# Optimization experiments

Measured on AMD Instinct MI355X. Metric: run time of the kernel, lower is better.

The kernel has to match this reference:

```python
import jax, jax.numpy as jnp
import numpy as np

STRIDE = 4
IMG_H, IMG_W = 800, 1216
NMS_THRESH = 0.7
PRE_NMS = 1000
POST_NMS = 1000
MIN_SIZE = 0.0
SCALE_CLAMP = float(np.log(1000.0 / 16.0))  # detectron2 Box2BoxTransform clamp
A = 3  # anchors per location


def _cell_anchors():
    size = 32.0
    ars = jnp.array([0.5, 1.0, 2.0], jnp.float32)
    area = size * size
    w = jnp.sqrt(area / ars)
    h = ars * w
    return jnp.stack([-w / 2, -h / 2, w / 2, h / 2], axis=1)  # [A,4]


def _anchors(H, W):
    sx = jnp.arange(W, dtype=jnp.float32) * STRIDE
    sy = jnp.arange(H, dtype=jnp.float32) * STRIDE
    gy, gx = jnp.meshgrid(sy, sx, indexing='ij')
    shifts = jnp.stack([gx, gy, gx, gy], axis=-1).reshape(-1, 1, 4)  # [H*W,1,4]
    return (shifts + _cell_anchors()[None]).reshape(-1, 4)  # [H*W*A,4]


def _conv(x, w, b, pad):
    y = jax.lax.conv_general_dilated(x, w, (1, 1), pad,
                                     dimension_numbers=('NCHW', 'OIHW', 'NCHW'))
    return y + b[None, :, None, None]


def _decode(anchors, deltas):
    # anchors [M,4], deltas [N,M,4]; weights (1,1,1,1)
    wa = anchors[:, 2] - anchors[:, 0]
    ha = anchors[:, 3] - anchors[:, 1]
    cx = anchors[:, 0] + 0.5 * wa
    cy = anchors[:, 1] + 0.5 * ha
    dx, dy = deltas[..., 0], deltas[..., 1]
    dw = jnp.minimum(deltas[..., 2], SCALE_CLAMP)
    dh = jnp.minimum(deltas[..., 3], SCALE_CLAMP)
    px = dx * wa + cx
    py = dy * ha + cy
    pw = jnp.exp(dw) * wa
    ph = jnp.exp(dh) * ha
    return jnp.stack([px - 0.5 * pw, py - 0.5 * ph,
                      px + 0.5 * pw, py + 0.5 * ph], axis=-1)


def _iou_matrix(boxes):  # [K,4] -> [K,K]
    area = (boxes[:, 2] - boxes[:, 0]) * (boxes[:, 3] - boxes[:, 1])
    lt = jnp.maximum(boxes[:, None, :2], boxes[None, :, :2])
    rb = jnp.minimum(boxes[:, None, 2:], boxes[None, :, 2:])
    wh = jnp.clip(rb - lt, 0.0)
    inter = wh[..., 0] * wh[..., 1]
    return inter / jnp.maximum(area[:, None] + area[None, :] - inter, 1e-9)


def _nms_keep(boxes):
    # boxes already sorted by descending score; greedy NMS
    iou = _iou_matrix(boxes)
    K = boxes.shape[0]

    def step(sup, i):
        keep = ~sup[i]
        sup = sup | (keep & (iou[i] > NMS_THRESH))
        return sup, keep

    _, keep = jax.lax.scan(step, jnp.zeros(K, bool), jnp.arange(K))
    return keep


def setup_inputs() -> dict:
    key = jax.random.key(0)
    ks = jax.random.split(key, 4)
    features = jax.random.normal(ks[0], (2, 256, 200, 304), jnp.float32)
    w_conv = jax.random.normal(ks[1], (256, 256, 3, 3), jnp.float32) * 0.01
    b_conv = jnp.zeros((256,), jnp.float32)
    w_obj = jax.random.normal(ks[2], (3, 256, 1, 1), jnp.float32) * 0.01
    b_obj = jnp.zeros((3,), jnp.float32)
    w_delta = jax.random.normal(ks[3], (12, 256, 1, 1), jnp.float32) * 0.01
    b_delta = jnp.zeros((12,), jnp.float32)
    return {"features": features, "w_conv": w_conv, "b_conv": b_conv,
            "w_obj": w_obj, "b_obj": b_obj, "w_delta": w_delta, "b_delta": b_delta}


def reference(features, w_conv, b_conv, w_obj, b_obj, w_delta, b_delta):
    N, C, H, W = features.shape
    t = jax.nn.relu(_conv(features, w_conv, b_conv, 'SAME'))
    logits = _conv(t, w_obj, b_obj, 'VALID')            # [N,A,H,W]
    deltas = _conv(t, w_delta, b_delta, 'VALID')        # [N,4A,H,W]
    logits = logits.transpose(0, 2, 3, 1).reshape(N, -1)               # [N,H*W*A]
    deltas = deltas.reshape(N, A, 4, H, W).transpose(0, 3, 4, 1, 2).reshape(N, -1, 4)

    anchors = _anchors(H, W)                             # [H*W*A,4]
    boxes = _decode(anchors, deltas)                     # [N,M,4]
    boxes = jnp.stack([jnp.clip(boxes[..., 0], 0.0, IMG_W),
                       jnp.clip(boxes[..., 1], 0.0, IMG_H),
                       jnp.clip(boxes[..., 2], 0.0, IMG_W),
                       jnp.clip(boxes[..., 3], 0.0, IMG_H)], axis=-1)

    valid = ((boxes[..., 2] - boxes[..., 0]) >= MIN_SIZE) & \
            ((boxes[..., 3] - boxes[..., 1]) >= MIN_SIZE)
    scores = jnp.where(valid, logits, -jnp.inf)

    top_s, top_i = jax.lax.top_k(scores, PRE_NMS)                      # sorted desc
    top_b = jnp.take_along_axis(boxes, top_i[..., None], axis=1)       # [N,K,4]

    keep = jax.vmap(_nms_keep)(top_b)                                  # [N,K]
    s = jnp.where(keep, top_s, -jnp.inf)
    fin_s, fin_i = jax.lax.top_k(s, POST_NMS)                          # sorted desc (=final sort)
    fin_b = jnp.take_along_axis(top_b, fin_i[..., None], axis=1)
    fin_b = jnp.where(jnp.isfinite(fin_s)[..., None], fin_b, 0.0)
    return fin_b, fin_s
```

## Files before the change

### kernel.cpp

```cpp
#include <hip/hip_runtime.h>
#include <math.h>
#include <stdint.h>

#define CC 256
#define HH 200
#define WW 304
#define NN 2
#define HW 60800
#define MM 182400
#define KK 1000
#define HP 202
#define WP 306
#define SCALE_CLAMP_F 4.135166556742356f
#define NEG_SENTINEL -1.0e30f
#define CAND_CAP 2048

typedef __attribute__((ext_vector_type(8))) short short8;
typedef __attribute__((ext_vector_type(4))) float f32x4;

__device__ __forceinline__ unsigned short f2bf(float f) {
  unsigned u = __float_as_uint(f);
  u += 0x7FFFu + ((u >> 16) & 1u);
  return (unsigned short)(u >> 16);
}
__device__ __forceinline__ unsigned int fkey(float s) {
  unsigned int u = __float_as_uint(s);
  return (u & 0x80000000u) ? ~u : (u | 0x80000000u);
}
__device__ __forceinline__ float iou_ref(float4 a, float4 b) {
#pragma clang fp contract(off)
  float areaA = (a.z - a.x) * (a.w - a.y);
  float areaB = (b.z - b.x) * (b.w - b.y);
  float ltx = fmaxf(a.x, b.x), lty = fmaxf(a.y, b.y);
  float rbx = fminf(a.z, b.z), rby = fminf(a.w, b.w);
  float w = fmaxf(rbx - ltx, 0.0f), h = fmaxf(rby - lty, 0.0f);
  float inter = w * h;
  float denom = fmaxf(areaA + areaB - inter, 1e-9f);
  return inter / denom;
}
__device__ __forceinline__ void gload16(const void* g, void* l) {
  __builtin_amdgcn_global_load_lds(
      (const __attribute__((address_space(1))) unsigned int*)g,
      (__attribute__((address_space(3))) unsigned int*)l, 16, 0, 0);
}
__device__ __forceinline__ int swz(int byte) {
  return byte ^ (((byte >> 7) & 7) << 4);
}
__device__ __forceinline__ short8 mk_b1(short8 v0, short8 v2, bool hi15) {
  union { short8 s; int i[4]; } a, c, o;
  a.s = v0; c.s = v2;
#pragma unroll
  for (int w = 0; w < 4; ++w) {
    int s = __builtin_amdgcn_mov_dpp(a.i[w], 0x111, 0xF, 0xF, true);
    int t = __builtin_amdgcn_mov_dpp(c.i[w], 0x101, 0xF, 0xF, true);
    o.i[w] = hi15 ? t : s;
  }
  return o.s;
}

__global__ __launch_bounds__(256) void pack_kernel(
    const float* __restrict__ w, unsigned short* __restrict__ wt_b,
    const float* __restrict__ in, unsigned short* __restrict__ fbp,
    unsigned int* __restrict__ ghist, unsigned int* __restrict__ cnt) {
  __shared__ unsigned short tile[64][65];
  int b = blockIdx.x;
  int tid = threadIdx.x;
  if (b < 2304) {
    int o = b * 256 + tid;
    int cin = o & 255, cout = (o >> 8) & 255, pos = o >> 16;
    wt_b[o] = f2bf(w[(cout * 256 + cin) * 9 + pos]);
  } else if (b < 10032) {
    int bb = b - 2304;
    int bx = bb % 966, rem = bb / 966;
    int by = rem & 3, n = rem >> 2;
    int p0 = bx * 64, c0 = by * 64;
    int lane = tid & 63;
    int p = p0 + lane;
    int yp = 0, xp = 0;
    bool inb = false;
    if (p < HP * WP) {
      yp = p / WP; xp = p - yp * WP;
      inb = (yp >= 1 && yp <= HH && xp >= 1 && xp <= WW);
    }
    for (int ci = tid >> 6; ci < 64; ci += 4) {
      float v = 0.f;
      if (inb) v = in[(((size_t)n * CC + c0 + ci) * HH + (yp - 1)) * WW + (xp - 1)];
      tile[ci][lane] = f2bf(v);
    }
    __syncthreads();
    for (int i = 0; i < 4; ++i) {
      int idx4 = (i * 256 + tid) * 4;
      int hwi = idx4 >> 6, cb = idx4 & 63;
      int pp = p0 + hwi;
      if (pp < HP * WP) {
        ushort4 v;
        v.x = tile[cb][hwi]; v.y = tile[cb + 1][hwi];
        v.z = tile[cb + 2][hwi]; v.w = tile[cb + 3][hwi];
        *(ushort4*)&fbp[((size_t)n * HP * WP + pp) * 256 + c0 + cb] = v;
      }
    }
  } else {
    int i = (b - 10032) * 256 + tid;
    ghist[i] = 0;
    if (i < 2) cnt[i] = 0;
  }
}

__global__ __launch_bounds__(256) void conv_mfma(
    const unsigned short* __restrict__ wt_b, const unsigned short* __restrict__ fbp,
    const float* __restrict__ bias, const float* __restrict__ w_obj,
    const float* __restrict__ w_delta, float* __restrict__ phead) {
  __shared__ __align__(16) unsigned short lA[2][12288];
  __shared__ __align__(16) unsigned short lB[2][5760];
  __shared__ float bl_l[128];
  int tid = threadIdx.x;
  int lane = tid & 63, wid = tid >> 6;
  int wm = wid >> 1, wn = wid & 1;
  int lrow = lane & 15, lgrp = lane >> 4;
  bool hi15 = (lrow == 15);
  int zz = blockIdx.z;
  int n = zz >> 1, ct = zz & 1;
  int X0 = blockIdx.x * 16, Y0 = blockIdx.y * 8;

  f32x4 acc[4][4];
#pragma unroll
  for (int m = 0; m < 4; ++m)
#pragma unroll
    for (int r = 0; r < 4; ++r) acc[m][r] = {0.f, 0.f, 0.f, 0.f};

  if (tid < 128) bl_l[tid] = bias[ct * 128 + tid];

  auto stageA3 = [&](int s, int buf) {
    int cc = s / 3, ky = s - cc * 3;
#pragma unroll
    for (int t = 0; t < 3; ++t) {
      int pos = ky * 3 + t;
#pragma unroll
      for (int is = 0; is < 2; ++is) {
        int idx = is * 256 + tid;
        int L = swz(idx * 16);
        int cout = L >> 6, q = (L >> 4) & 3;
        const unsigned short* g =
            wt_b + (((size_t)pos * 256 + ct * 128 + cout) << 8) + cc * 32 + q * 8;
        gload16(g, (char*)&lA[buf][0] + t * 8192 + is * 4096 + (wid << 10));
      }
    }
  };
  auto stageB = [&](int cc, int buf) {
#pragma unroll
    for (int is = 0; is < 3; ++is) {
      int idx = is * 256 + tid;
      if (idx < 720) {
        int L = swz(idx * 16);
        int rc = L >> 6, q = (L >> 4) & 3;
        int row = rc / 18, col = rc - row * 18;
        const unsigned short* g =
            fbp + (((size_t)n * HP + Y0 + row) * WP + X0 + col) * 256 + cc * 32 + q * 8;
        gload16(g, (char*)&lB[buf][0] + is * 4096 + (wid << 10));
      }
    }
  };

  stageA3(0, 0);
  stageB(0, 0);
  __syncthreads();

#pragma unroll 1
  for (int s = 0; s < 24; ++s) {
    int cc = s / 3, ky = s - cc * 3;
    int bb = cc & 1;
    if (s < 23) stageA3(s + 1, (s + 1) & 1);
    if (ky == 0 && cc < 7) stageB(cc + 1, bb ^ 1);

    short8 b0[4], b2[4];
#pragma unroll
    for (int r = 0; r < 4; ++r) {
      int row = wn * 4 + r + ky;
      int Lb0 = ((row * 18 + lrow) << 6) + (lgrp << 4);
      int Lb2 = ((row * 18 + lrow + 2) << 6) + (lgrp << 4);
      b0[r] = *(const short8*)((const char*)&lB[bb][0] + swz(Lb0));
      b2[r] = *(const short8*)((const char*)&lB[bb][0] + swz(Lb2));
    }
#pragma unroll
    for (int kx = 0; kx < 3; ++kx) {
      short8 af[4];
#pragma unroll
      for (int m = 0; m < 4; ++m) {
        int Lb = ((wm * 64 + m * 16 + lrow) << 6) + (lgrp << 4);
        af[m] = *(const short8*)((const char*)&lA[s & 1][0] + kx * 8192 + swz(Lb));
      }
      short8 bsel[4];
#pragma unroll
      for (int r = 0; r < 4; ++r)
        bsel[r] = (kx == 0) ? b0[r] : (kx == 2) ? b2[r] : mk_b1(b0[r], b2[r], hi15);
#pragma unroll
      for (int m = 0; m < 4; ++m)
#pragma unroll
        for (int r = 0; r < 4; ++r)
          acc[m][r] =
              __builtin_amdgcn_mfma_f32_16x16x32_bf16(af[m], bsel[r], acc[m][r], 0, 0, 0);
    }
    __syncthreads();
  }

#pragma unroll
  for (int m = 0; m < 4; ++m)
#pragma unroll
    for (int j = 0; j < 4; ++j) {
      float b = bl_l[wm * 64 + m * 16 + (lgrp << 2) + j];
#pragma unroll
      for (int r = 0; r < 4; ++r) acc[m][r][j] = fmaxf(acc[m][r][j] + b, 0.f);
    }

  float* whl_l = (float*)&lA[0][0];
  for (int i = tid; i < 1920; i += 256) {
    int o = i >> 7, cl = i & 127;
    whl_l[i] = (o < 3) ? w_obj[o * 256 + ct * 128 + cl]
                       : w_delta[(o - 3) * 256 + ct * 128 + cl];
  }
  __syncthreads();

  float* hacc = (float*)&lB[0][0];
#pragma unroll 1
  for (int o = 0; o < 15; ++o) {
    float p0 = 0.f, p1 = 0.f, p2 = 0.f, p3 = 0.f;
#pragma unroll
    for (int m = 0; m < 4; ++m)
#pragma unroll
      for (int j = 0; j < 4; ++j) {
        float w = whl_l[o * 128 + wm * 64 + m * 16 + (lgrp << 2) + j];
        p0 = fmaf(w, acc[m][0][j], p0);
        p1 = fmaf(w, acc[m][1][j], p1);
        p2 = fmaf(w, acc[m][2][j], p2);
        p3 = fmaf(w, acc[m][3][j], p3);
      }
    p0 += __shfl_xor(p0, 16); p0 += __shfl_xor(p0, 32);
    p1 += __shfl_xor(p1, 16); p1 += __shfl_xor(p1, 32);
    p2 += __shfl_xor(p2, 16); p2 += __shfl_xor(p2, 32);
    p3 += __shfl_xor(p3, 16); p3 += __shfl_xor(p3, 32);
    if (lgrp == 0) {
      hacc[(((o * 8) + wn * 4 + 0) * 16 + lrow) * 2 + wm] = p0;
      hacc[(((o * 8) + wn * 4 + 1) * 16 + lrow) * 2 + wm] = p1;
      hacc[(((o * 8) + wn * 4 + 2) * 16 + lrow) * 2 + wm] = p2;
      hacc[(((o * 8) + wn * 4 + 3) * 16 + lrow) * 2 + wm] = p3;
    }
  }
  __syncthreads();

  if (tid < 128) {
    int row = tid >> 4, col = tid & 15;
    int loc = (Y0 + row) * WW + (X0 + col);
    size_t base = ((size_t)zz * 15) * HW + loc;
#pragma unroll
    for (int o = 0; o < 15; ++o) {
      const float* hp = &hacc[((o * 8 + row) * 16 + col) * 2];
      phead[base + (size_t)o * HW] = hp[0] + hp[1];
    }
  }
}

__global__ __launch_bounds__(256) void decode_kernel(
    const float* __restrict__ phead, const float* __restrict__ b_obj,
    const float* __restrict__ b_delta, float* __restrict__ scores,
    float* __restrict__ boxes, unsigned long long* __restrict__ keys,
    unsigned int* __restrict__ ghist) {
  __shared__ unsigned int hl[8192];
  int tid = threadIdx.x;
  for (int i = tid; i < 8192; i += 256) hl[i] = 0;
  __syncthreads();
  int n = blockIdx.y;
  int loc = blockIdx.x * 256 + tid;
  if (loc < HW) {
    float ho[15];
    const float* p0 = phead + ((size_t)(n * 2 + 0) * 15) * HW + loc;
    const float* p1 = phead + ((size_t)(n * 2 + 1) * 15) * HW + loc;
#pragma unroll
    for (int o = 0; o < 15; ++o) ho[o] = p0[(size_t)o * HW] + p1[(size_t)o * HW];
#pragma unroll
    for (int o = 0; o < 3; ++o) ho[o] += b_obj[o];
#pragma unroll
    for (int o = 0; o < 12; ++o) ho[3 + o] += b_delta[o];
    {
#pragma clang fp contract(off)
      int h = loc / WW, w = loc - h * WW;
      float gx = (float)(w * 4);
      float gy = (float)(h * 4);
      float s2048 = sqrtf(2048.0f), s512 = sqrtf(512.0f);
      float aw[3] = {s2048, 32.0f, s512};
      float ah[3] = {0.5f * s2048, 32.0f, 2.0f * s512};
#pragma unroll
      for (int a = 0; a < 3; ++a) {
        float ax1 = gx - 0.5f * aw[a], ay1 = gy - 0.5f * ah[a];
        float ax2 = gx + 0.5f * aw[a], ay2 = gy + 0.5f * ah[a];
        float wa = ax2 - ax1, ha = ay2 - ay1;
        float cx = ax1 + 0.5f * wa, cy = ay1 + 0.5f * ha;
        float dx = ho[3 + a * 4 + 0], dy = ho[3 + a * 4 + 1];
        float dw = fminf(ho[3 + a * 4 + 2], SCALE_CLAMP_F);
        float dh = fminf(ho[3 + a * 4 + 3], SCALE_CLAMP_F);
        float px = dx * wa + cx, py = dy * ha + cy;
        float pw = expf(dw) * wa, ph = expf(dh) * ha;
        float x1 = px - 0.5f * pw, y1 = py - 0.5f * ph;
        float x2v = px + 0.5f * pw, y2v = py + 0.5f * ph;
        x1 = fminf(fmaxf(x1, 0.f), 1216.f);
        y1 = fminf(fmaxf(y1, 0.f), 800.f);
        x2v = fminf(fmaxf(x2v, 0.f), 1216.f);
        y2v = fminf(fmaxf(y2v, 0.f), 800.f);
        int m = loc * 3 + a;
        ((float4*)boxes)[(size_t)n * MM + m] = make_float4(x1, y1, x2v, y2v);
        float sc = ho[a];
        scores[(size_t)n * MM + m] = sc;
        unsigned long long k =
            ((unsigned long long)fkey(sc) << 18) | (unsigned long long)(262143 - m);
        keys[(size_t)n * MM + m] = k;
        atomicAdd(&hl[(unsigned)(k >> 37)], 1u);
      }
    }
  }
  __syncthreads();
  for (int i = tid; i < 8192; i += 256) {
    unsigned v = hl[i];
    if (v) atomicAdd(&ghist[n * 8192 + i], v);
  }
}

__global__ __launch_bounds__(256) void gather_kernel(
    const unsigned long long* __restrict__ keys, const unsigned int* __restrict__ ghist,
    unsigned int* __restrict__ cnt, unsigned long long* __restrict__ cand) {
  __shared__ unsigned int ps[256];
  __shared__ int bsh;
  int n = blockIdx.y, tid = threadIdx.x;
  const unsigned int* h = ghist + n * 8192;
  unsigned s = 0;
  for (int k = 0; k < 32; ++k) s += h[tid * 32 + k];
  ps[tid] = s;
  __syncthreads();
  if (tid == 0) {
    unsigned cum = 0; int b = 0;
    for (int t = 255; t >= 0; --t) {
      if (cum + ps[t] >= KK) {
        for (int bin = t * 32 + 31; bin >= t * 32; --bin) {
          cum += h[bin];
          if (cum >= KK) { b = bin; break; }
        }
        break;
      }
      cum += ps[t];
    }
    bsh = b;
  }
  __syncthreads();
  int b = bsh;
  const unsigned long long* kp = keys + (size_t)n * MM;
  int i0 = blockIdx.x * 2850, i1 = min(i0 + 2850, MM);
  for (int i = i0 + tid; i < i1; i += 256) {
    unsigned long long k = kp[i];
    if ((int)(unsigned)(k >> 37) >= b) {
      unsigned pos = atomicAdd(&cnt[n], 1u);
      if (pos < CAND_CAP) cand[(size_t)n * CAND_CAP + pos] = k;
    }
  }
}

__global__ __launch_bounds__(1024) void final_select(
    const unsigned long long* __restrict__ cand, const unsigned int* __restrict__ cnt,
    const float* __restrict__ scores, const float* __restrict__ boxes,
    float* __restrict__ s_scores, float* __restrict__ s_boxes) {
  __shared__ unsigned long long sel[CAND_CAP];
  int n = blockIdx.x, tid = threadIdx.x;
  int E = (int)min(cnt[n], (unsigned)CAND_CAP);
  for (int i = tid; i < CAND_CAP; i += 1024)
    sel[i] = (i < E) ? cand[(size_t)n * CAND_CAP + i] : 0ull;
  __syncthreads();
  for (unsigned k2 = 2; k2 <= CAND_CAP; k2 <<= 1) {
    for (unsigned j = k2 >> 1; j > 0; j >>= 1) {
      for (int i = tid; i < CAND_CAP; i += 1024) {
        int l = i ^ (int)j;
        if (l > i) {
          unsigned long long a = sel[i], bb = sel[l];
          bool sw = ((i & k2) == 0) ? (a < bb) : (a > bb);
          if (sw) { sel[i] = bb; sel[l] = a; }
        }
      }
      __syncthreads();
    }
  }
  if (tid < KK) {
    unsigned long long k = sel[tid];
    int m = 262143 - (int)(k & 0x3FFFFull);
    s_scores[n * KK + tid] = scores[(size_t)n * MM + m];
    ((float4*)s_boxes)[n * KK + tid] = ((const float4*)boxes)[(size_t)n * MM + m];
  }
}

__global__ __launch_bounds__(256) void mask_kernel(const float* __restrict__ s_boxes,
                                                   unsigned long long* __restrict__ mask) {
  int i = blockIdx.x, n = blockIdx.y;
  int tid = threadIdx.x, w = tid >> 6, lane = tid & 63;
  const float4* bp = (const float4*)s_boxes + n * KK;
  float4 bi = bp[i];
#pragma unroll
  for (int p = 0; p < 4; ++p) {
    int word = p * 4 + w;
    int j = word * 64 + lane;
    bool over = false;
    if (j < KK) {
      float4 bj = bp[j];
      over = iou_ref(bi, bj) > 0.7f;
    }
    unsigned long long bal = __ballot(over);
    if (lane == 0) mask[((size_t)n * KK + i) * 16 + word] = bal;
  }
}

__global__ __launch_bounds__(1024) void scan_write_kernel(
    const float* __restrict__ s_scores, const float* __restrict__ s_boxes,
    const unsigned long long* __restrict__ mask, float* __restrict__ out) {
  int n = blockIdx.x, tid = threadIdx.x;
  int wid = tid >> 6, lane = tid & 63;
  __shared__ unsigned long long swl[16];
  __shared__ unsigned long long keepw[16];
  __shared__ unsigned int wpre[17];
  if (tid < 16) swl[tid] = 0ull;
  __syncthreads();
  const unsigned long long* mrow = mask + (size_t)n * 16000;
  for (int c = 0; c < 16; ++c) {
    int i = c * 64 + lane;
    unsigned long long myword = (i < KK) ? mrow[(size_t)i * 16 + wid] : 0ull;
    if (wid == 0) {
      unsigned long long m = (i < KK) ? mrow[(size_t)i * 16 + c] : 0ull;
      unsigned long long cur = swl[c];
      unsigned long long kw = 0ull;
      int lim = min(64, KK - c * 64);
      for (int b = 0; b < lim; ++b) {
        unsigned long long mb = __shfl(m, b);
        if (!((cur >> b) & 1ull)) { kw |= (1ull << b); cur |= mb; }
      }
      if (lane == 0) keepw[c] = kw;
    }
    __syncthreads();
    unsigned long long kw = keepw[c];
    unsigned long long v = ((kw >> lane) & 1ull) ? myword : 0ull;
#pragma unroll
    for (int s = 32; s > 0; s >>= 1) v |= __shfl_xor(v, s);
    if (lane == 0) swl[wid] |= v;
    __syncthreads();
  }
  if (tid == 0) {
    unsigned int c = 0;
    for (int w2 = 0; w2 < 16; ++w2) { wpre[w2] = c; c += (unsigned int)__popcll(keepw[w2]); }
    wpre[16] = c;
  }
  __syncthreads();
  if (tid < KK) {
    int word = tid >> 6, bit = tid & 63;
    unsigned long long kwv = keepw[word];
    bool kept = (kwv >> bit) & 1ull;
    unsigned int before = wpre[word] + (unsigned int)__popcll(kwv & ((1ull << bit) - 1ull));
    unsigned int nk = wpre[16];
    unsigned int dst = kept ? before : nk + ((unsigned int)tid - before);
    float4 b = kept ? ((const float4*)s_boxes)[n * KK + tid] : make_float4(0.f, 0.f, 0.f, 0.f);
    float s = kept ? s_scores[n * KK + tid] : NEG_SENTINEL;
    ((float4*)out)[n * KK + dst] = b;
    out[8000 + n * KK + dst] = s;
  }
}

extern "C" void kernel_launch(void* const* d_in, const int* in_sizes, int n_in,
                              void* d_out, int out_size, void* d_ws, size_t ws_size,
                              hipStream_t stream) {
  (void)in_sizes; (void)n_in; (void)out_size; (void)ws_size;
  const float* features = (const float*)d_in[0];
  const float* w_conv   = (const float*)d_in[1];
  const float* b_conv   = (const float*)d_in[2];
  const float* w_obj    = (const float*)d_in[3];
  const float* b_obj    = (const float*)d_in[4];
  const float* w_delta  = (const float*)d_in[5];
  const float* b_delta  = (const float*)d_in[6];

  char* ws = (char*)d_ws;
  unsigned short* wt_b = (unsigned short*)ws;
  unsigned short* fbp  = (unsigned short*)(ws + 1179648);
  char* O = ws + 64475136;
  float* phead = (float*)O;
  float* scores = (float*)(O + 14592000);
  float* boxes  = (float*)(O + 16051200);
  unsigned long long* keys = (unsigned long long*)(O + 21888000);
  char* P = O + 24806400;
  unsigned int* ghist = (unsigned int*)P;
  unsigned int* cnt = (unsigned int*)(P + 65536);
  unsigned long long* cand = (unsigned long long*)(P + 65792);
  float* s_scores = (float*)(P + 98560);
  float* s_boxes  = (float*)(P + 106752);
  unsigned long long* maskbuf = (unsigned long long*)(P + 139264);
  float* out = (float*)d_out;

  pack_kernel<<<10096, 256, 0, stream>>>(w_conv, wt_b, features, fbp, ghist, cnt);
  conv_mfma<<<dim3(19, 25, 4), 256, 0, stream>>>(wt_b, fbp, b_conv, w_obj, w_delta, phead);
  decode_kernel<<<dim3(238, 2), 256, 0, stream>>>(phead, b_obj, b_delta,
                                                  scores, boxes, keys, ghist);
  gather_kernel<<<dim3(64, 2), 256, 0, stream>>>(keys, ghist, cnt, cand);
  final_select<<<2, 1024, 0, stream>>>(cand, cnt, scores, boxes, s_scores, s_boxes);
  mask_kernel<<<dim3(1000, 2), 256, 0, stream>>>(s_boxes, maskbuf);
  scan_write_kernel<<<2, 1024, 0, stream>>>(s_scores, s_boxes, maskbuf, out);
}
```

Measured before the change: 374.9 us.

## Fuse post-conv tail kernels into one cooperative kernel with grid syncs

```diff
diff --git a/kernel.cpp b/kernel.cpp
--- a/kernel.cpp
+++ b/kernel.cpp
@@ -1,4 +1,5 @@
 #include <hip/hip_runtime.h>
+#include <hip/hip_cooperative_groups.h>
 #include <math.h>
 #include <stdint.h>
 
@@ -14,6 +15,8 @@
 #define SCALE_CLAMP_F 4.135166556742356f
 #define NEG_SENTINEL -1.0e30f
 #define CAND_CAP 2048
+
+namespace cg = cooperative_groups;
 
 typedef __attribute__((ext_vector_type(8))) short short8;
 typedef __attribute__((ext_vector_type(4))) float f32x4;
@@ -259,209 +262,209 @@
   }
 }
 
-__global__ __launch_bounds__(256) void decode_kernel(
+__global__ __launch_bounds__(1024) void tail_kernel(
     const float* __restrict__ phead, const float* __restrict__ b_obj,
     const float* __restrict__ b_delta, float* __restrict__ scores,
     float* __restrict__ boxes, unsigned long long* __restrict__ keys,
-    unsigned int* __restrict__ ghist) {
-  __shared__ unsigned int hl[8192];
-  int tid = threadIdx.x;
-  for (int i = tid; i < 8192; i += 256) hl[i] = 0;
-  __syncthreads();
-  int n = blockIdx.y;
-  int loc = blockIdx.x * 256 + tid;
-  if (loc < HW) {
-    float ho[15];
-    const float* p0 = phead + ((size_t)(n * 2 + 0) * 15) * HW + loc;
-    const float* p1 = phead + ((size_t)(n * 2 + 1) * 15) * HW + loc;
-#pragma unroll
-    for (int o = 0; o < 15; ++o) ho[o] = p0[(size_t)o * HW] + p1[(size_t)o * HW];
-#pragma unroll
-    for (int o = 0; o < 3; ++o) ho[o] += b_obj[o];
-#pragma unroll
-    for (int o = 0; o < 12; ++o) ho[3 + o] += b_delta[o];
-    {
-#pragma clang fp contract(off)
-      int h = loc / WW, w = loc - h * WW;
-      float gx = (float)(w * 4);
-      float gy = (float)(h * 4);
-      float s2048 = sqrtf(2048.0f), s512 = sqrtf(512.0f);
-      float aw[3] = {s2048, 32.0f, s512};
-      float ah[3] = {0.5f * s2048, 32.0f, 2.0f * s512};
-#pragma unroll
-      for (int a = 0; a < 3; ++a) {
-        float ax1 = gx - 0.5f * aw[a], ay1 = gy - 0.5f * ah[a];
-        float ax2 = gx + 0.5f * aw[a], ay2 = gy + 0.5f * ah[a];
-        float wa = ax2 - ax1, ha = ay2 - ay1;
-        float cx = ax1 + 0.5f * wa, cy = ay1 + 0.5f * ha;
-        float dx = ho[3 + a * 4 + 0], dy = ho[3 + a * 4 + 1];
-        float dw = fminf(ho[3 + a * 4 + 2], SCALE_CLAMP_F);
-        float dh = fminf(ho[3 + a * 4 + 3], SCALE_CLAMP_F);
-        float px = dx * wa + cx, py = dy * ha + cy;
-        float pw = expf(dw) * wa, ph = expf(dh) * ha;
-        float x1 = px - 0.5f * pw, y1 = py - 0.5f * ph;
-        float x2v = px + 0.5f * pw, y2v = py + 0.5f * ph;
-        x1 = fminf(fmaxf(x1, 0.f), 1216.f);
-        y1 = fminf(fmaxf(y1, 0.f), 800.f);
-        x2v = fminf(fmaxf(x2v, 0.f), 1216.f);
-        y2v = fminf(fmaxf(y2v, 0.f), 800.f);
-        int m = loc * 3 + a;
-        ((float4*)boxes)[(size_t)n * MM + m] = make_float4(x1, y1, x2v, y2v);
-        float sc = ho[a];
-        scores[(size_t)n * MM + m] = sc;
-        unsigned long long k =
-            ((unsigned long long)fkey(sc) << 18) | (unsigned long long)(262143 - m);
-        keys[(size_t)n * MM + m] = k;
-        atomicAdd(&hl[(unsigned)(k >> 37)], 1u);
-      }
-    }
-  }
-  __syncthreads();
-  for (int i = tid; i < 8192; i += 256) {
-    unsigned v = hl[i];
-    if (v) atomicAdd(&ghist[n * 8192 + i], v);
-  }
-}
-
-__global__ __launch_bounds__(256) void gather_kernel(
-    const unsigned long long* __restrict__ keys, const unsigned int* __restrict__ ghist,
-    unsigned int* __restrict__ cnt, unsigned long long* __restrict__ cand) {
+    unsigned int* __restrict__ ghist, unsigned int* __restrict__ cnt,
+    unsigned long long* __restrict__ cand, float* __restrict__ s_scores,
+    float* __restrict__ s_boxes, unsigned long long* __restrict__ maskbuf,
+    float* __restrict__ out) {
+  cg::grid_group grid = cg::this_grid();
+  __shared__ __align__(16) char smem[32768];
   __shared__ unsigned int ps[256];
   __shared__ int bsh;
-  int n = blockIdx.y, tid = threadIdx.x;
-  const unsigned int* h = ghist + n * 8192;
-  unsigned s = 0;
-  for (int k = 0; k < 32; ++k) s += h[tid * 32 + k];
-  ps[tid] = s;
-  __syncthreads();
-  if (tid == 0) {
-    unsigned cum = 0; int b = 0;
-    for (int t = 255; t >= 0; --t) {
-      if (cum + ps[t] >= KK) {
-        for (int bin = t * 32 + 31; bin >= t * 32; --bin) {
-          cum += h[bin];
-          if (cum >= KK) { b = bin; break; }
-        }
-        break;
-      }
-      cum += ps[t];
-    }
-    bsh = b;
-  }
-  __syncthreads();
-  int b = bsh;
-  const unsigned long long* kp = keys + (size_t)n * MM;
-  int i0 = blockIdx.x * 2850, i1 = min(i0 + 2850, MM);
-  for (int i = i0 + tid; i < i1; i += 256) {
-    unsigned long long k = kp[i];
-    if ((int)(unsigned)(k >> 37) >= b) {
-      unsigned pos = atomicAdd(&cnt[n], 1u);
-      if (pos < CAND_CAP) cand[(size_t)n * CAND_CAP + pos] = k;
-    }
-  }
-}
-
-__global__ __launch_bounds__(1024) void final_select(
-    const unsigned long long* __restrict__ cand, const unsigned int* __restrict__ cnt,
-    const float* __restrict__ scores, const float* __restrict__ boxes,
-    float* __restrict__ s_scores, float* __restrict__ s_boxes) {
-  __shared__ unsigned long long sel[CAND_CAP];
-  int n = blockIdx.x, tid = threadIdx.x;
-  int E = (int)min(cnt[n], (unsigned)CAND_CAP);
-  for (int i = tid; i < CAND_CAP; i += 1024)
-    sel[i] = (i < E) ? cand[(size_t)n * CAND_CAP + i] : 0ull;
-  __syncthreads();
-  for (unsigned k2 = 2; k2 <= CAND_CAP; k2 <<= 1) {
-    for (unsigned j = k2 >> 1; j > 0; j >>= 1) {
-      for (int i = tid; i < CAND_CAP; i += 1024) {
-        int l = i ^ (int)j;
-        if (l > i) {
-          unsigned long long a = sel[i], bb = sel[l];
-          bool sw = ((i & k2) == 0) ? (a < bb) : (a > bb);
-          if (sw) { sel[i] = bb; sel[l] = a; }
-        }
-      }
-      __syncthreads();
-    }
-  }
-  if (tid < KK) {
-    unsigned long long k = sel[tid];
-    int m = 262143 - (int)(k & 0x3FFFFull);
-    s_scores[n * KK + tid] = scores[(size_t)n * MM + m];
-    ((float4*)s_boxes)[n * KK + tid] = ((const float4*)boxes)[(size_t)n * MM + m];
-  }
-}
-
-__global__ __launch_bounds__(256) void mask_kernel(const float* __restrict__ s_boxes,
-                                                   unsigned long long* __restrict__ mask) {
-  int i = blockIdx.x, n = blockIdx.y;
-  int tid = threadIdx.x, w = tid >> 6, lane = tid & 63;
-  const float4* bp = (const float4*)s_boxes + n * KK;
-  float4 bi = bp[i];
-#pragma unroll
-  for (int p = 0; p < 4; ++p) {
-    int word = p * 4 + w;
-    int j = word * 64 + lane;
-    bool over = false;
-    if (j < KK) {
-      float4 bj = bp[j];
-      over = iou_ref(bi, bj) > 0.7f;
-    }
-    unsigned long long bal = __ballot(over);
-    if (lane == 0) mask[((size_t)n * KK + i) * 16 + word] = bal;
-  }
-}
-
-__global__ __launch_bounds__(1024) void scan_write_kernel(
-    const float* __restrict__ s_scores, const float* __restrict__ s_boxes,
-    const unsigned long long* __restrict__ mask, float* __restrict__ out) {
-  int n = blockIdx.x, tid = threadIdx.x;
-  int wid = tid >> 6, lane = tid & 63;
   __shared__ unsigned long long swl[16];
   __shared__ unsigned long long keepw[16];
   __shared__ unsigned int wpre[17];
-  if (tid < 16) swl[tid] = 0ull;
+  int b = blockIdx.x, tid = threadIdx.x;
+  int nb = b / 60, bx = b - nb * 60;
+
+  unsigned int* hl = (unsigned int*)smem;
+  for (int i = tid; i < 8192; i += 1024) hl[i] = 0;
   __syncthreads();
-  const unsigned long long* mrow = mask + (size_t)n * 16000;
-  for (int c = 0; c < 16; ++c) {
-    int i = c * 64 + lane;
-    unsigned long long myword = (i < KK) ? mrow[(size_t)i * 16 + wid] : 0ull;
-    if (wid == 0) {
-      unsigned long long m = (i < KK) ? mrow[(size_t)i * 16 + c] : 0ull;
-      unsigned long long cur = swl[c];
-      unsigned long long kw = 0ull;
-      int lim = min(64, KK - c * 64);
-      for (int b = 0; b < lim; ++b) {
-        unsigned long long mb = __shfl(m, b);
-        if (!((cur >> b) & 1ull)) { kw |= (1ull << b); cur |= mb; }
-      }
-      if (lane == 0) keepw[c] = kw;
-    }
-    __syncthreads();
-    unsigned long long kw = keepw[c];
-    unsigned long long v = ((kw >> lane) & 1ull) ? myword : 0ull;
-#pragma unroll
-    for (int s = 32; s > 0; s >>= 1) v |= __shfl_xor(v, s);
-    if (lane == 0) swl[wid] |= v;
-    __syncthreads();
-  }
-  if (tid == 0) {
-    unsigned int c = 0;
-    for (int w2 = 0; w2 < 16; ++w2) { wpre[w2] = c; c += (unsigned int)__popcll(keepw[w2]); }
-    wpre[16] = c;
+  {
+    int loc = bx * 1024 + tid;
+    if (loc < HW) {
+      float ho[15];
+      const float* p0 = phead + ((size_t)(nb * 2 + 0) * 15) * HW + loc;
+      const float* p1 = phead + ((size_t)(nb * 2 + 1) * 15) * HW + loc;
+#pragma unroll
+      for (int o = 0; o < 15; ++o) ho[o] = p0[(size_t)o * HW] + p1[(size_t)o * HW];
+#pragma unroll
+      for (int o = 0; o < 3; ++o) ho[o] += b_obj[o];
+#pragma unroll
+      for (int o = 0; o < 12; ++o) ho[3 + o] += b_delta[o];
+      {
+#pragma clang fp contract(off)
+        int h = loc / WW, w = loc - h * WW;
+        float gx = (float)(w * 4);
+        float gy = (float)(h * 4);
+        float s2048 = sqrtf(2048.0f), s512 = sqrtf(512.0f);
+        float aw[3] = {s2048, 32.0f, s512};
+        float ah[3] = {0.5f * s2048, 32.0f, 2.0f * s512};
+#pragma unroll
+        for (int a = 0; a < 3; ++a) {
+          float ax1 = gx - 0.5f * aw[a], ay1 = gy - 0.5f * ah[a];
+          float ax2 = gx + 0.5f * aw[a], ay2 = gy + 0.5f * ah[a];
+          float wa = ax2 - ax1, ha = ay2 - ay1;
+          float cx = ax1 + 0.5f * wa, cy = ay1 + 0.5f * ha;
+          float dx = ho[3 + a * 4 + 0], dy = ho[3 + a * 4 + 1];
+          float dw = fminf(ho[3 + a * 4 + 2], SCALE_CLAMP_F);
+          float dh = fminf(ho[3 + a * 4 + 3], SCALE_CLAMP_F);
+          float px = dx * wa + cx, py = dy * ha + cy;
+          float pw = expf(dw) * wa, ph = expf(dh) * ha;
+          float x1 = px - 0.5f * pw, y1 = py - 0.5f * ph;
+          float x2v = px + 0.5f * pw, y2v = py + 0.5f * ph;
+          x1 = fminf(fmaxf(x1, 0.f), 1216.f);
+          y1 = fminf(fmaxf(y1, 0.f), 800.f);
+          x2v = fminf(fmaxf(x2v, 0.f), 1216.f);
+          y2v = fminf(fmaxf(y2v, 0.f), 800.f);
+          int m = loc * 3 + a;
+          ((float4*)boxes)[(size_t)nb * MM + m] = make_float4(x1, y1, x2v, y2v);
+          float sc = ho[a];
+          scores[(size_t)nb * MM + m] = sc;
+          unsigned long long k =
+              ((unsigned long long)fkey(sc) << 18) | (unsigned long long)(262143 - m);
+          keys[(size_t)nb * MM + m] = k;
+          atomicAdd(&hl[(unsigned)(k >> 37)], 1u);
+        }
+      }
+    }
   }
   __syncthreads();
-  if (tid < KK) {
-    int word = tid >> 6, bit = tid & 63;
-    unsigned long long kwv = keepw[word];
-    bool kept = (kwv >> bit) & 1ull;
-    unsigned int before = wpre[word] + (unsigned int)__popcll(kwv & ((1ull << bit) - 1ull));
-    unsigned int nk = wpre[16];
-    unsigned int dst = kept ? before : nk + ((unsigned int)tid - before);
-    float4 b = kept ? ((const float4*)s_boxes)[n * KK + tid] : make_float4(0.f, 0.f, 0.f, 0.f);
-    float s = kept ? s_scores[n * KK + tid] : NEG_SENTINEL;
-    ((float4*)out)[n * KK + dst] = b;
-    out[8000 + n * KK + dst] = s;
+  for (int i = tid; i < 8192; i += 1024) {
+    unsigned v = hl[i];
+    if (v) atomicAdd(&ghist[nb * 8192 + i], v);
+  }
+  grid.sync();
+
+  {
+    const unsigned int* h = ghist + nb * 8192;
+    if (tid < 256) {
+      unsigned s = 0;
+      for (int k = 0; k < 32; ++k) s += h[tid * 32 + k];
+      ps[tid] = s;
+    }
+    __syncthreads();
+    if (tid == 0) {
+      unsigned cum = 0; int bbin = 0;
+      for (int t = 255; t >= 0; --t) {
+        if (cum + ps[t] >= KK) {
+          for (int bin = t * 32 + 31; bin >= t * 32; --bin) {
+            cum += h[bin];
+            if (cum >= KK) { bbin = bin; break; }
+          }
+          break;
+        }
+        cum += ps[t];
+      }
+      bsh = bbin;
+    }
+    __syncthreads();
+    int thr = bsh;
+    const unsigned long long* kp = keys + (size_t)nb * MM;
+    int i0 = bx * 3040, i1 = min(i0 + 3040, MM);
+    for (int i = i0 + tid; i < i1; i += 1024) {
+      unsigned long long k = kp[i];
+      if ((int)(unsigned)(k >> 37) >= thr) {
+        unsigned pos = atomicAdd(&cnt[nb], 1u);
+        if (pos < CAND_CAP) cand[(size_t)nb * CAND_CAP + pos] = k;
+      }
+    }
+  }
+  grid.sync();
+
+  if (b < 2) {
+    int n = b;
+    unsigned long long* sel = (unsigned long long*)smem;
+    int E = (int)min(cnt[n], (unsigned)CAND_CAP);
+    for (int i = tid; i < CAND_CAP; i += 1024)
+      sel[i] = (i < E) ? cand[(size_t)n * CAND_CAP + i] : 0ull;
+    __syncthreads();
+    for (unsigned k2 = 2; k2 <= CAND_CAP; k2 <<= 1) {
+      for (unsigned j = k2 >> 1; j > 0; j >>= 1) {
+        for (int i = tid; i < CAND_CAP; i += 1024) {
+          int l = i ^ (int)j;
+          if (l > i) {
+            unsigned long long a = sel[i], bb2 = sel[l];
+            bool sw = ((i & k2) == 0) ? (a < bb2) : (a > bb2);
+            if (sw) { sel[i] = bb2; sel[l] = a; }
+          }
+        }
+        __syncthreads();
+      }
+    }
+    if (tid < KK) {
+      unsigned long long k = sel[tid];
+      int m = 262143 - (int)(k & 0x3FFFFull);
+      s_scores[n * KK + tid] = scores[(size_t)n * MM + m];
+      ((float4*)s_boxes)[n * KK + tid] = ((const float4*)boxes)[(size_t)n * MM + m];
+    }
+  }
+  grid.sync();
+
+  {
+    int word = tid >> 6, lane = tid & 63;
+    for (int flat = b; flat < 2 * KK; flat += 120) {
+      int n = flat / KK, i = flat - n * KK;
+      const float4* bp = (const float4*)s_boxes + n * KK;
+      float4 bi = bp[i];
+      int j = tid;
+      bool over = false;
+      if (j < KK) over = iou_ref(bi, bp[j]) > 0.7f;
+      unsigned long long bal = __ballot(over);
+      if (lane == 0) maskbuf[((size_t)n * KK + i) * 16 + word] = bal;
+    }
+  }
+  grid.sync();
+
+  if (b < 2) {
+    int n = b;
+    int wid = tid >> 6, lane = tid & 63;
+    if (tid < 16) swl[tid] = 0ull;
+    __syncthreads();
+    const unsigned long long* mrow = maskbuf + (size_t)n * 16000;
+    for (int c = 0; c < 16; ++c) {
+      int i = c * 64 + lane;
+      unsigned long long myword = (i < KK) ? mrow[(size_t)i * 16 + wid] : 0ull;
+      if (wid == 0) {
+        unsigned long long m = (i < KK) ? mrow[(size_t)i * 16 + c] : 0ull;
+        unsigned long long cur = swl[c];
+        unsigned long long kw = 0ull;
+        int lim = min(64, KK - c * 64);
+        for (int bbit = 0; bbit < lim; ++bbit) {
+          unsigned long long mb = __shfl(m, bbit);
+          if (!((cur >> bbit) & 1ull)) { kw |= (1ull << bbit); cur |= mb; }
+        }
+        if (lane == 0) keepw[c] = kw;
+      }
+      __syncthreads();
+      unsigned long long kw = keepw[c];
+      unsigned long long v = ((kw >> lane) & 1ull) ? myword : 0ull;
+#pragma unroll
+      for (int s = 32; s > 0; s >>= 1) v |= __shfl_xor(v, s);
+      if (lane == 0) swl[wid] |= v;
+      __syncthreads();
+    }
+    if (tid == 0) {
+      unsigned int c = 0;
+      for (int w2 = 0; w2 < 16; ++w2) { wpre[w2] = c; c += (unsigned int)__popcll(keepw[w2]); }
+      wpre[16] = c;
+    }
+    __syncthreads();
+    if (tid < KK) {
+      int word = tid >> 6, bit = tid & 63;
+      unsigned long long kwv = keepw[word];
+      bool kept = (kwv >> bit) & 1ull;
+      unsigned int before = wpre[word] + (unsigned int)__popcll(kwv & ((1ull << bit) - 1ull));
+      unsigned int nk = wpre[16];
+      unsigned int dst = kept ? before : nk + ((unsigned int)tid - before);
+      float4 bb3 = kept ? ((const float4*)s_boxes)[n * KK + tid] : make_float4(0.f, 0.f, 0.f, 0.f);
+      float s = kept ? s_scores[n * KK + tid] : NEG_SENTINEL;
+      ((float4*)out)[n * KK + dst] = bb3;
+      out[8000 + n * KK + dst] = s;
+    }
   }
 }
 
@@ -496,10 +499,10 @@
 
   pack_kernel<<<10096, 256, 0, stream>>>(w_conv, wt_b, features, fbp, ghist, cnt);
   conv_mfma<<<dim3(19, 25, 4), 256, 0, stream>>>(wt_b, fbp, b_conv, w_obj, w_delta, phead);
-  decode_kernel<<<dim3(238, 2), 256, 0, stream>>>(phead, b_obj, b_delta,
-                                                  scores, boxes, keys, ghist);
-  gather_kernel<<<dim3(64, 2), 256, 0, stream>>>(keys, ghist, cnt, cand);
-  final_select<<<2, 1024, 0, stream>>>(cand, cnt, scores, boxes, s_scores, s_boxes);
-  mask_kernel<<<dim3(1000, 2), 256, 0, stream>>>(s_boxes, maskbuf);
-  scan_write_kernel<<<2, 1024, 0, stream>>>(s_scores, s_boxes, maskbuf, out);
-}
+
+  void* args[] = {(void*)&phead, (void*)&b_obj, (void*)&b_delta, (void*)&scores,
+                  (void*)&boxes, (void*)&keys, (void*)&ghist, (void*)&cnt,
+                  (void*)&cand, (void*)&s_scores, (void*)&s_boxes, (void*)&maskbuf,
+                  (void*)&out};
+  hipLaunchCooperativeKernel((void*)tail_kernel, dim3(120), dim3(1024), args, 0, stream);
+}
```

New measurement: 422.2 us. 1.13x slower.
